# Optimization experiments

Hardware: AMD Instinct MI355X
Metric: run time of the kernel (lower is better)

## Reference

```python
import jax, jax.numpy as jnp
import numpy as np
from functools import partial

HID = 256
HOR = 5

def _lin(k, i, o):
    return jax.random.normal(k, (i, o), jnp.float32) / np.sqrt(i)

def setup_inputs() -> dict:
    key = jax.random.key(0)
    ks = jax.random.split(key, 32)
    B, T, D, Hf, Wf = 4, 16, 768, 16, 16
    H, W = 1024, 1024
    inp = {}
    inp['features'] = jax.random.normal(ks[0], (B, T, D, Hf, Wf), jnp.float32)
    inp['predictions'] = jax.random.uniform(ks[1], (B, T, 1, H, W), dtype=jnp.float32)
    # position encoder: 4 -> HID -> HID
    inp['pe_w1'] = _lin(ks[2], 4, HID); inp['pe_b1'] = jnp.zeros((HID,), jnp.float32)
    inp['pe_w2'] = _lin(ks[3], HID, HID); inp['pe_b2'] = jnp.zeros((HID,), jnp.float32)
    # 2-layer LSTM, gate order i,f,g,o (torch convention)
    inp['wih0'] = _lin(ks[4], HID, 4 * HID); inp['whh0'] = _lin(ks[5], HID, 4 * HID)
    inp['bih0'] = jnp.zeros((4 * HID,), jnp.float32); inp['bhh0'] = jnp.zeros((4 * HID,), jnp.float32)
    inp['wih1'] = _lin(ks[6], HID, 4 * HID); inp['whh1'] = _lin(ks[7], HID, 4 * HID)
    inp['bih1'] = jnp.zeros((4 * HID,), jnp.float32); inp['bhh1'] = jnp.zeros((4 * HID,), jnp.float32)
    # motion predictor: HID -> HID -> HID/2 -> HOR*4
    inp['mp_w1'] = _lin(ks[8], HID, HID); inp['mp_b1'] = jnp.zeros((HID,), jnp.float32)
    inp['mp_w2'] = _lin(ks[9], HID, HID // 2); inp['mp_b2'] = jnp.zeros((HID // 2,), jnp.float32)
    inp['mp_w3'] = _lin(ks[10], HID // 2, HOR * 4); inp['mp_b3'] = jnp.zeros((HOR * 4,), jnp.float32)
    # confidence: HID -> HID/2 -> HOR
    inp['cf_w1'] = _lin(ks[11], HID, HID // 2); inp['cf_b1'] = jnp.zeros((HID // 2,), jnp.float32)
    inp['cf_w2'] = _lin(ks[12], HID // 2, HOR); inp['cf_b2'] = jnp.zeros((HOR,), jnp.float32)
    return inp

def _extract_bboxes(predictions):
    # predictions: (B,T,1,H,W) -> bboxes (B,T,4) in (cx,cy,w,h), normalized
    B, T, _, H, W = predictions.shape
    mask = predictions[:, :, 0] > 0.5  # (B,T,H,W)
    xs = jnp.arange(W, dtype=jnp.float32)           # (W,)
    ys = jnp.arange(H, dtype=jnp.float32)[:, None]  # (H,1)
    big = jnp.float32(H + W)
    x_min = jnp.min(jnp.where(mask, xs, big), axis=(-2, -1))
    x_max = jnp.max(jnp.where(mask, xs, -1.0), axis=(-2, -1))
    y_min = jnp.min(jnp.where(mask, ys, big), axis=(-2, -1))
    y_max = jnp.max(jnp.where(mask, ys, -1.0), axis=(-2, -1))
    has = jnp.any(mask, axis=(-2, -1))  # (B,T)
    cx = (x_min + x_max) / 2.0 / W
    cy = (y_min + y_max) / 2.0 / H
    w = (x_max - x_min) / W
    h = (y_max - y_min) / H
    bbox = jnp.stack([cx, cy, w, h], axis=-1)  # (B,T,4)
    default = jnp.array([0.5, 0.5, 0.1, 0.1], dtype=jnp.float32)
    return jnp.where(has[..., None], bbox, default)

def _lstm_layer(x, wih, whh, bih, bhh):
    # x: (B,T,HID); returns (hs (B,T,H), h_final (B,H))
    B = x.shape[0]
    xg = jnp.einsum('bti,ig->btg', x, wih) + bih  # (B,T,4H)
    def step(carry, xg_t):
        h, c = carry
        g = xg_t + h @ whh + bhh
        i, f, gg, o = jnp.split(g, 4, axis=-1)
        i = jax.nn.sigmoid(i); f = jax.nn.sigmoid(f)
        gg = jnp.tanh(gg); o = jax.nn.sigmoid(o)
        c = f * c + i * gg
        h = o * jnp.tanh(c)
        return (h, c), h
    z = jnp.zeros((B, HID), x.dtype)
    (h, c), hs = jax.lax.scan(step, (z, z), xg.swapaxes(0, 1))
    return hs.swapaxes(0, 1), h

def reference(features, predictions, pe_w1, pe_b1, pe_w2, pe_b2,
              wih0, whh0, bih0, bhh0, wih1, whh1, bih1, bhh1,
              mp_w1, mp_b1, mp_w2, mp_b2, mp_w3, mp_b3,
              cf_w1, cf_b1, cf_w2, cf_b2):
    B, T = features.shape[:2]
    bboxes = _extract_bboxes(predictions)  # (B,T,4)
    pos = jax.nn.relu(bboxes @ pe_w1 + pe_b1)
    pos = jax.nn.relu(pos @ pe_w2 + pe_b2)  # (B,T,HID)
    h1, _ = _lstm_layer(pos, wih0, whh0, bih0, bhh0)
    motion_features, last_hidden = _lstm_layer(h1, wih1, whh1, bih1, bhh1)
    x = jax.nn.relu(last_hidden @ mp_w1 + mp_b1)
    x = jax.nn.relu(x @ mp_w2 + mp_b2)
    predicted_deltas = (x @ mp_w3 + mp_b3).reshape(B, HOR, 4)
    last_bbox = bboxes[:, -1:, :]
    predicted_bboxes = last_bbox + jnp.cumsum(predicted_deltas, axis=1)
    c = jax.nn.relu(last_hidden @ cf_w1 + cf_b1)
    confidence = jax.nn.sigmoid(c @ cf_w2 + cf_b2)  # (B,HOR)
    predicted_locations = predicted_bboxes[..., :2]
    predicted_scales = predicted_bboxes[..., 2:]
    return (predicted_deltas, predicted_bboxes, predicted_locations,
            predicted_scales, motion_features, confidence, bboxes)
```

## Files before the change

### kernel.cpp

```cpp
#include <hip/hip_runtime.h>
#include <math.h>

#define BIGI (1 << 30)

#define PM_OFF    0
#define MM_OFF    8192
#define FLAGS_OFF 8448
#define POS2_OFF  8512
#define H1S_OFF   24896
#define H2_OFF    41280

#define OUT_DELTAS 0
#define OUT_PBB    80
#define OUT_LOC    160
#define OUT_SCL    200
#define OUT_MF     240
#define OUT_CONF   16624
#define OUT_BBOX   16644

__device__ __forceinline__ float sigmoidf_(float x) { return 1.0f / (1.0f + expf(-x)); }

__device__ __forceinline__ void cstoref(float* p, float v) {
    __hip_atomic_store(p, v, __ATOMIC_RELAXED, __HIP_MEMORY_SCOPE_AGENT);
}
__device__ __forceinline__ float cloadf(const float* p) {
    return __hip_atomic_load(p, __ATOMIC_RELAXED, __HIP_MEMORY_SCOPE_AGENT);
}
__device__ __forceinline__ int cloadi(const int* p) {
    return __hip_atomic_load(p, __ATOMIC_RELAXED, __HIP_MEMORY_SCOPE_AGENT);
}

__device__ __forceinline__ void pollf(const int* fl, int target) {
    if (threadIdx.x == 0) {
        for (;;) {
            int m = cloadi(fl + 0);
            m = min(m, cloadi(fl + 1)); m = min(m, cloadi(fl + 2));
            m = min(m, cloadi(fl + 3)); m = min(m, cloadi(fl + 4));
            m = min(m, cloadi(fl + 5)); m = min(m, cloadi(fl + 6));
            m = min(m, cloadi(fl + 7));
            if (m >= target) break;
            __builtin_amdgcn_s_sleep(2);
        }
    }
    __syncthreads();
}

__global__ __launch_bounds__(256) void k_minmax(const float4* __restrict__ pred,
                                                int* __restrict__ pm) {
    int img = blockIdx.x >> 5;
    int chunk = blockIdx.x & 31;
    int tid = threadIdx.x;
    int base = img * 262144 + chunk * 8192 + tid;
    int xmn = BIGI, xmx = -1, ymn = BIGI, ymx = -1;
#pragma unroll 4
    for (int i = 0; i < 32; ++i) {
        int idx4 = base + i * 256;
        float4 v = pred[idx4];
        int x = (idx4 << 2) & 1023;
        int y = (idx4 >> 8) & 1023;
        bool m0 = v.x > 0.5f, m1 = v.y > 0.5f, m2 = v.z > 0.5f, m3 = v.w > 0.5f;
        int cmn = m0 ? x : (m1 ? x + 1 : (m2 ? x + 2 : (m3 ? x + 3 : BIGI)));
        int cmx = m3 ? x + 3 : (m2 ? x + 2 : (m1 ? x + 1 : (m0 ? x : -1)));
        xmn = min(xmn, cmn);
        xmx = max(xmx, cmx);
        if (m0 | m1 | m2 | m3) { ymn = min(ymn, y); ymx = max(ymx, y); }
    }
    for (int off = 32; off > 0; off >>= 1) {
        xmn = min(xmn, __shfl_down(xmn, off));
        xmx = max(xmx, __shfl_down(xmx, off));
        ymn = min(ymn, __shfl_down(ymn, off));
        ymx = max(ymx, __shfl_down(ymx, off));
    }
    __shared__ int red[4][4];
    int wave = tid >> 6;
    if ((tid & 63) == 0) { red[0][wave] = xmn; red[1][wave] = xmx; red[2][wave] = ymn; red[3][wave] = ymx; }
    __syncthreads();
    if (tid == 0) {
        xmn = min(min(red[0][0], red[0][1]), min(red[0][2], red[0][3]));
        xmx = max(max(red[1][0], red[1][1]), max(red[1][2], red[1][3]));
        ymn = min(min(red[2][0], red[2][1]), min(red[2][2], red[2][3]));
        ymx = max(max(red[3][0], red[3][1]), max(red[3][2], red[3][3]));
        ((int4*)pm)[blockIdx.x] = make_int4(xmn, xmx, ymn, ymx);
    }
}

__global__ __launch_bounds__(256) void k_prep(const int* __restrict__ pm,
    int* __restrict__ mm, int* __restrict__ flags,
    const float* __restrict__ pe_w1, const float* __restrict__ pe_b1,
    const float* __restrict__ pe_w2, const float* __restrict__ pe_b2,
    float* __restrict__ pos2, float* __restrict__ out) {
    __shared__ float bb[4];
    __shared__ float p1[256];
    int w = blockIdx.x, tid = threadIdx.x;
    if (w == 0 && tid < 64) flags[tid] = 0;
    if (tid < 64) {
        int xmn = BIGI, xmx = -1, ymn = BIGI, ymx = -1;
        if (tid < 32) {
            int4 v = ((const int4*)pm)[w * 32 + tid];
            xmn = v.x; xmx = v.y; ymn = v.z; ymx = v.w;
        }
        for (int off = 32; off > 0; off >>= 1) {
            xmn = min(xmn, __shfl_down(xmn, off));
            xmx = max(xmx, __shfl_down(xmx, off));
            ymn = min(ymn, __shfl_down(ymn, off));
            ymx = max(ymx, __shfl_down(ymx, off));
        }
        if (tid == 0) {
            mm[w * 4 + 0] = xmn; mm[w * 4 + 1] = xmx;
            mm[w * 4 + 2] = ymn; mm[w * 4 + 3] = ymx;
            float cx, cy, bw, bh;
            if (xmx >= 0) {
                cx = (float)(xmn + xmx) * (0.5f / 1024.0f);
                cy = (float)(ymn + ymx) * (0.5f / 1024.0f);
                bw = (float)(xmx - xmn) * (1.0f / 1024.0f);
                bh = (float)(ymx - ymn) * (1.0f / 1024.0f);
            } else { cx = 0.5f; cy = 0.5f; bw = 0.1f; bh = 0.1f; }
            bb[0] = cx; bb[1] = cy; bb[2] = bw; bb[3] = bh;
            out[OUT_BBOX + w * 4 + 0] = cx; out[OUT_BBOX + w * 4 + 1] = cy;
            out[OUT_BBOX + w * 4 + 2] = bw; out[OUT_BBOX + w * 4 + 3] = bh;
        }
    }
    __syncthreads();
    {
        float v = bb[0] * pe_w1[tid] + bb[1] * pe_w1[256 + tid] +
                  bb[2] * pe_w1[512 + tid] + bb[3] * pe_w1[768 + tid] + pe_b1[tid];
        p1[tid] = fmaxf(v, 0.0f);
    }
    __syncthreads();
    float acc = pe_b2[tid];
#pragma unroll 4
    for (int k = 0; k < 256; ++k) acc += p1[k] * pe_w2[k * 256 + tid];
    pos2[w * 256 + tid] = fmaxf(acc, 0.0f);
}

__global__ __launch_bounds__(256, 1) void k_lstm(
    const float* __restrict__ wih0, const float* __restrict__ whh0,
    const float* __restrict__ bih0, const float* __restrict__ bhh0,
    const float* __restrict__ wih1, const float* __restrict__ whh1,
    const float* __restrict__ bih1, const float* __restrict__ bhh1,
    const float* __restrict__ mp_w1, const float* __restrict__ mp_b1,
    const float* __restrict__ mp_w2, const float* __restrict__ mp_b2,
    const float* __restrict__ mp_w3, const float* __restrict__ mp_b3,
    const float* __restrict__ cf_w1, const float* __restrict__ cf_b1,
    const float* __restrict__ cf_w2, const float* __restrict__ cf_b2,
    const float* __restrict__ pos2, float* __restrict__ h1s,
    float* __restrict__ h2, int* __restrict__ flags,
    const int* __restrict__ mm, float* __restrict__ out) {
    __shared__ float px[4096];
    __shared__ float partX[4096];
    __shared__ float xgl[2048];
    __shared__ float hsm[256];
    __shared__ float part[256];
    __shared__ float gatesL[128];
    const int tid = threadIdx.x;
    const int b = blockIdx.x >> 3, g = blockIdx.x & 7;
    const int j = tid & 127, kh = tid >> 7;
    const int col = ((j >> 5) << 8) + g * 32 + (j & 31);
    int* flb = flags + b * 16;
    float4 wreg[32];

    for (int layer = 0; layer < 2; ++layer) {
        const float* wih = layer ? wih1 : wih0;
        const float* whh = layer ? whh1 : whh0;
        const float* bih = layer ? bih1 : bih0;
        const float* bhh = layer ? bhh1 : bhh0;

        if (layer == 0) {
            for (int i = tid; i < 4096; i += 256) px[i] = pos2[b * 4096 + i];
        } else {
            pollf(flb, 16);
            for (int i = tid; i < 4096; i += 256) px[i] = cloadf(&h1s[b * 4096 + i]);
        }
#pragma unroll
        for (int k4 = 0; k4 < 32; ++k4) {
            int r = kh * 128 + k4 * 4;
            wreg[k4].x = wih[(r + 0) * 1024 + col];
            wreg[k4].y = wih[(r + 1) * 1024 + col];
            wreg[k4].z = wih[(r + 2) * 1024 + col];
            wreg[k4].w = wih[(r + 3) * 1024 + col];
        }
        __syncthreads();
        for (int t = 0; t < 16; ++t) {
            float a = 0.0f;
            const float4* p4 = (const float4*)&px[t * 256 + kh * 128];
#pragma unroll
            for (int k4 = 0; k4 < 32; ++k4) {
                float4 h4 = p4[k4];
                a += h4.x * wreg[k4].x + h4.y * wreg[k4].y + h4.z * wreg[k4].z + h4.w * wreg[k4].w;
            }
            partX[kh * 2048 + t * 128 + j] = a;
        }
        __syncthreads();
        {
            float bsum = bih[col] + bhh[col];
            int t0 = tid >> 7;
            for (int i = 0; i < 8; ++i) {
                int t = t0 + 2 * i;
                xgl[t * 128 + j] = partX[t * 128 + j] + partX[2048 + t * 128 + j] + bsum;
            }
        }
#pragma unroll
        for (int k4 = 0; k4 < 32; ++k4) {
            int r = kh * 128 + k4 * 4;
            wreg[k4].x = whh[(r + 0) * 1024 + col];
            wreg[k4].y = whh[(r + 1) * 1024 + col];
            wreg[k4].z = whh[(r + 2) * 1024 + col];
            wreg[k4].w = whh[(r + 3) * 1024 + col];
        }
        __syncthreads();

        float cst = 0.0f;
        for (int t = 0; t < 16; ++t) {
            if (t) {
                pollf(flb, layer * 16 + t);
                hsm[tid] = (layer == 0)
                    ? cloadf(&h1s[(b * 16 + t - 1) * 256 + tid])
                    : cloadf(&h2[b * 512 + ((t - 1) & 1) * 256 + tid]);
            }
            __syncthreads();
            float a = 0.0f;
            if (t) {
                const float4* h4p = (const float4*)&hsm[kh * 128];
#pragma unroll
                for (int k4 = 0; k4 < 32; ++k4) {
                    float4 h4 = h4p[k4];
                    a += h4.x * wreg[k4].x + h4.y * wreg[k4].y + h4.z * wreg[k4].z + h4.w * wreg[k4].w;
                }
            }
            part[tid] = a;
            __syncthreads();
            if (tid < 128) gatesL[tid] = part[tid] + part[128 + tid] + xgl[t * 128 + tid];
            __syncthreads();
            if (tid < 32) {
                float gi = gatesL[tid], gf = gatesL[32 + tid];
                float gg = gatesL[64 + tid], go = gatesL[96 + tid];
                float i_ = sigmoidf_(gi), f_ = sigmoidf_(gf);
                float g_ = tanhf(gg), o_ = sigmoidf_(go);
                cst = f_ * cst + i_ * g_;
                float h = o_ * tanhf(cst);
                int unit = g * 32 + tid;
                if (layer == 0) {
                    cstoref(&h1s[(b * 16 + t) * 256 + unit], h);
                } else {
                    cstoref(&h2[b * 512 + (t & 1) * 256 + unit], h);
                    out[OUT_MF + (b * 16 + t) * 256 + unit] = h;
                }
            }
            __syncthreads();
            if (tid == 0)
                __hip_atomic_store(&flb[g], layer * 16 + t + 1,
                                   __ATOMIC_RELAXED, __HIP_MEMORY_SCOPE_AGENT);
        }
    }

    if (g != 0) return;
    pollf(flb, 32);
    float* lh = px;
    float* x1 = px + 256;
    float* c1 = px + 512;
    float* x2 = px + 768;
    float* dl = px + 896;
    lh[tid] = cloadf(&h2[b * 512 + 256 + tid]);
    __syncthreads();
    {
        float a = mp_b1[tid];
#pragma unroll 4
        for (int k = 0; k < 256; ++k) a += lh[k] * mp_w1[k * 256 + tid];
        x1[tid] = fmaxf(a, 0.0f);
    }
    if (tid < 128) {
        float a = cf_b1[tid];
#pragma unroll 4
        for (int k = 0; k < 256; ++k) a += lh[k] * cf_w1[k * 128 + tid];
        c1[tid] = fmaxf(a, 0.0f);
    }
    __syncthreads();
    if (tid < 128) {
        float a = mp_b2[tid];
#pragma unroll 4
        for (int k = 0; k < 256; ++k) a += x1[k] * mp_w2[k * 128 + tid];
        x2[tid] = fmaxf(a, 0.0f);
    } else if (tid < 133) {
        int jj = tid - 128;
        float a = cf_b2[jj];
#pragma unroll 4
        for (int k = 0; k < 128; ++k) a += c1[k] * cf_w2[k * 5 + jj];
        out[OUT_CONF + b * 5 + jj] = sigmoidf_(a);
    }
    __syncthreads();
    if (tid < 20) {
        float a = mp_b3[tid];
#pragma unroll 4
        for (int k = 0; k < 128; ++k) a += x2[k] * mp_w3[k * 20 + tid];
        dl[tid] = a;
        out[OUT_DELTAS + b * 20 + tid] = a;
    }
    __syncthreads();
    if (tid < 4) {
        int img = b * 16 + 15;
        int xmn = mm[img * 4 + 0], xmx = mm[img * 4 + 1];
        int ymn = mm[img * 4 + 2], ymx = mm[img * 4 + 3];
        float v;
        if (xmx >= 0) {
            if (tid == 0)      v = (float)(xmn + xmx) * (0.5f / 1024.0f);
            else if (tid == 1) v = (float)(ymn + ymx) * (0.5f / 1024.0f);
            else if (tid == 2) v = (float)(xmx - xmn) * (1.0f / 1024.0f);
            else               v = (float)(ymx - ymn) * (1.0f / 1024.0f);
        } else v = (tid < 2) ? 0.5f : 0.1f;
        float acc = v;
        for (int hh = 0; hh < 5; ++hh) {
            acc += dl[hh * 4 + tid];
            out[OUT_PBB + b * 20 + hh * 4 + tid] = acc;
            if (tid < 2) out[OUT_LOC + b * 10 + hh * 2 + tid] = acc;
            else out[OUT_SCL + b * 10 + hh * 2 + (tid - 2)] = acc;
        }
    }
}

extern "C" void kernel_launch(void* const* d_in, const int* in_sizes, int n_in,
                              void* d_out, int out_size, void* d_ws, size_t ws_size,
                              hipStream_t stream) {
    (void)in_sizes; (void)n_in; (void)out_size; (void)ws_size;
    const float* pred = (const float*)d_in[1];
    const float* pe_w1 = (const float*)d_in[2];
    const float* pe_b1 = (const float*)d_in[3];
    const float* pe_w2 = (const float*)d_in[4];
    const float* pe_b2 = (const float*)d_in[5];
    const float* wih0 = (const float*)d_in[6];
    const float* whh0 = (const float*)d_in[7];
    const float* bih0 = (const float*)d_in[8];
    const float* bhh0 = (const float*)d_in[9];
    const float* wih1 = (const float*)d_in[10];
    const float* whh1 = (const float*)d_in[11];
    const float* bih1 = (const float*)d_in[12];
    const float* bhh1 = (const float*)d_in[13];
    const float* mp_w1 = (const float*)d_in[14];
    const float* mp_b1 = (const float*)d_in[15];
    const float* mp_w2 = (const float*)d_in[16];
    const float* mp_b2 = (const float*)d_in[17];
    const float* mp_w3 = (const float*)d_in[18];
    const float* mp_b3 = (const float*)d_in[19];
    const float* cf_w1 = (const float*)d_in[20];
    const float* cf_b1 = (const float*)d_in[21];
    const float* cf_w2 = (const float*)d_in[22];
    const float* cf_b2 = (const float*)d_in[23];
    float* out = (float*)d_out;
    int* wsi = (int*)d_ws;
    float* wsf = (float*)d_ws;

    hipLaunchKernelGGL(k_minmax, dim3(64 * 32), dim3(256), 0, stream,
                       (const float4*)pred, wsi + PM_OFF);
    hipLaunchKernelGGL(k_prep, dim3(64), dim3(256), 0, stream,
                       wsi + PM_OFF, wsi + MM_OFF, wsi + FLAGS_OFF,
                       pe_w1, pe_b1, pe_w2, pe_b2,
                       wsf + POS2_OFF, out);
    hipLaunchKernelGGL(k_lstm, dim3(32), dim3(256), 0, stream,
                       wih0, whh0, bih0, bhh0,
                       wih1, whh1, bih1, bhh1,
                       mp_w1, mp_b1, mp_w2, mp_b2, mp_w3, mp_b3,
                       cf_w1, cf_b1, cf_w2, cf_b2,
                       wsf + POS2_OFF, wsf + H1S_OFF, wsf + H2_OFF,
                       wsi + FLAGS_OFF, wsi + MM_OFF, out);
}
```

Baseline: 681.7 us.

## Replace per-block flag polling with tagged 64-bit hidden-state words

Inter-block synchronization in the recurrent LSTM no longer uses separate per-group progress flags. Each hidden value is written as one 64-bit word that packs the value with a step tag, and consumers spin on each word until the tag matches. This removes the extra __syncthreads and flag store per step, and the single-thread poll followed by a barrier before the loads. In exchange every thread polls its own word, the zeroing of the larger tagged buffer moves into the prep kernel, and hidden-state traffic doubles in size.

New measurement: 658.2 us. 3.5% less time.

```diff
diff --git a/kernel.cpp b/kernel.cpp
--- a/kernel.cpp
+++ b/kernel.cpp
@@ -5,10 +5,10 @@
 
 #define PM_OFF    0
 #define MM_OFF    8192
-#define FLAGS_OFF 8448
-#define POS2_OFF  8512
-#define H1S_OFF   24896
-#define H2_OFF    41280
+#define POS2_OFF  8448
+#define HT0_OFF   24832
+#define HT2_OFF   57600
+#define HT_WORDS  36864
 
 #define OUT_DELTAS 0
 #define OUT_PBB    80
@@ -20,29 +20,18 @@
 
 __device__ __forceinline__ float sigmoidf_(float x) { return 1.0f / (1.0f + expf(-x)); }
 
-__device__ __forceinline__ void cstoref(float* p, float v) {
+__device__ __forceinline__ void storeh(unsigned long long* p, float h, int tag) {
+    unsigned long long v =
+        ((unsigned long long)(unsigned)tag << 32) | (unsigned long long)__float_as_uint(h);
     __hip_atomic_store(p, v, __ATOMIC_RELAXED, __HIP_MEMORY_SCOPE_AGENT);
 }
-__device__ __forceinline__ float cloadf(const float* p) {
-    return __hip_atomic_load(p, __ATOMIC_RELAXED, __HIP_MEMORY_SCOPE_AGENT);
-}
-__device__ __forceinline__ int cloadi(const int* p) {
-    return __hip_atomic_load(p, __ATOMIC_RELAXED, __HIP_MEMORY_SCOPE_AGENT);
-}
-
-__device__ __forceinline__ void pollf(const int* fl, int target) {
-    if (threadIdx.x == 0) {
-        for (;;) {
-            int m = cloadi(fl + 0);
-            m = min(m, cloadi(fl + 1)); m = min(m, cloadi(fl + 2));
-            m = min(m, cloadi(fl + 3)); m = min(m, cloadi(fl + 4));
-            m = min(m, cloadi(fl + 5)); m = min(m, cloadi(fl + 6));
-            m = min(m, cloadi(fl + 7));
-            if (m >= target) break;
-            __builtin_amdgcn_s_sleep(2);
-        }
-    }
-    __syncthreads();
+__device__ __forceinline__ float pollh(const unsigned long long* p, int tag) {
+    unsigned long long v = __hip_atomic_load(p, __ATOMIC_RELAXED, __HIP_MEMORY_SCOPE_AGENT);
+    while ((int)(v >> 32) != tag) {
+        __builtin_amdgcn_s_sleep(1);
+        v = __hip_atomic_load(p, __ATOMIC_RELAXED, __HIP_MEMORY_SCOPE_AGENT);
+    }
+    return __uint_as_float((unsigned)v);
 }
 
 __global__ __launch_bounds__(256) void k_minmax(const float4* __restrict__ pred,
@@ -85,14 +74,14 @@
 }
 
 __global__ __launch_bounds__(256) void k_prep(const int* __restrict__ pm,
-    int* __restrict__ mm, int* __restrict__ flags,
+    int* __restrict__ mm, int* __restrict__ ht,
     const float* __restrict__ pe_w1, const float* __restrict__ pe_b1,
     const float* __restrict__ pe_w2, const float* __restrict__ pe_b2,
     float* __restrict__ pos2, float* __restrict__ out) {
     __shared__ float bb[4];
     __shared__ float p1[256];
     int w = blockIdx.x, tid = threadIdx.x;
-    if (w == 0 && tid < 64) flags[tid] = 0;
+    for (int i = w * 256 + tid; i < HT_WORDS; i += 64 * 256) ht[i] = 0;
     if (tid < 64) {
         int xmn = BIGI, xmx = -1, ymn = BIGI, ymx = -1;
         if (tid < 32) {
@@ -143,8 +132,8 @@
     const float* __restrict__ mp_w3, const float* __restrict__ mp_b3,
     const float* __restrict__ cf_w1, const float* __restrict__ cf_b1,
     const float* __restrict__ cf_w2, const float* __restrict__ cf_b2,
-    const float* __restrict__ pos2, float* __restrict__ h1s,
-    float* __restrict__ h2, int* __restrict__ flags,
+    const float* __restrict__ pos2, unsigned long long* __restrict__ hT0,
+    unsigned long long* __restrict__ hT2,
     const int* __restrict__ mm, float* __restrict__ out) {
     __shared__ float px[4096];
     __shared__ float partX[4096];
@@ -156,7 +145,6 @@
     const int b = blockIdx.x >> 3, g = blockIdx.x & 7;
     const int j = tid & 127, kh = tid >> 7;
     const int col = ((j >> 5) << 8) + g * 32 + (j & 31);
-    int* flb = flags + b * 16;
     float4 wreg[32];
 
     for (int layer = 0; layer < 2; ++layer) {
@@ -168,8 +156,10 @@
         if (layer == 0) {
             for (int i = tid; i < 4096; i += 256) px[i] = pos2[b * 4096 + i];
         } else {
-            pollf(flb, 16);
-            for (int i = tid; i < 4096; i += 256) px[i] = cloadf(&h1s[b * 4096 + i]);
+            for (int i = tid; i < 4096; i += 256) {
+                int t = i >> 8, unit = i & 255;
+                px[i] = pollh(&hT0[((b * 16 + t) << 8) + unit], t + 1);
+            }
         }
 #pragma unroll
         for (int k4 = 0; k4 < 32; ++k4) {
@@ -212,10 +202,10 @@
         float cst = 0.0f;
         for (int t = 0; t < 16; ++t) {
             if (t) {
-                pollf(flb, layer * 16 + t);
-                hsm[tid] = (layer == 0)
-                    ? cloadf(&h1s[(b * 16 + t - 1) * 256 + tid])
-                    : cloadf(&h2[b * 512 + ((t - 1) & 1) * 256 + tid]);
+                const unsigned long long* src = (layer == 0)
+                    ? &hT0[((b * 16 + (t - 1)) << 8) + tid]
+                    : &hT2[(((b << 1) | ((t - 1) & 1)) << 8) + tid];
+                hsm[tid] = pollh(src, layer * 16 + t);
             }
             __syncthreads();
             float a = 0.0f;
@@ -239,28 +229,25 @@
                 cst = f_ * cst + i_ * g_;
                 float h = o_ * tanhf(cst);
                 int unit = g * 32 + tid;
+                int tag = layer * 16 + t + 1;
                 if (layer == 0) {
-                    cstoref(&h1s[(b * 16 + t) * 256 + unit], h);
+                    storeh(&hT0[((b * 16 + t) << 8) + unit], h, tag);
                 } else {
-                    cstoref(&h2[b * 512 + (t & 1) * 256 + unit], h);
+                    storeh(&hT2[(((b << 1) | (t & 1)) << 8) + unit], h, tag);
                     out[OUT_MF + (b * 16 + t) * 256 + unit] = h;
                 }
             }
-            __syncthreads();
-            if (tid == 0)
-                __hip_atomic_store(&flb[g], layer * 16 + t + 1,
-                                   __ATOMIC_RELAXED, __HIP_MEMORY_SCOPE_AGENT);
         }
     }
 
     if (g != 0) return;
-    pollf(flb, 32);
+    __syncthreads();
     float* lh = px;
     float* x1 = px + 256;
     float* c1 = px + 512;
     float* x2 = px + 768;
     float* dl = px + 896;
-    lh[tid] = cloadf(&h2[b * 512 + 256 + tid]);
+    lh[tid] = pollh(&hT2[((b << 1) | 1) << 8 | tid], 32);
     __syncthreads();
     {
         float a = mp_b1[tid];
@@ -351,7 +338,7 @@
     hipLaunchKernelGGL(k_minmax, dim3(64 * 32), dim3(256), 0, stream,
                        (const float4*)pred, wsi + PM_OFF);
     hipLaunchKernelGGL(k_prep, dim3(64), dim3(256), 0, stream,
-                       wsi + PM_OFF, wsi + MM_OFF, wsi + FLAGS_OFF,
+                       wsi + PM_OFF, wsi + MM_OFF, wsi + HT0_OFF,
                        pe_w1, pe_b1, pe_w2, pe_b2,
                        wsf + POS2_OFF, out);
     hipLaunchKernelGGL(k_lstm, dim3(32), dim3(256), 0, stream,
@@ -359,6 +346,8 @@
                        wih1, whh1, bih1, bhh1,
                        mp_w1, mp_b1, mp_w2, mp_b2, mp_w3, mp_b3,
                        cf_w1, cf_b1, cf_w2, cf_b2,
-                       wsf + POS2_OFF, wsf + H1S_OFF, wsf + H2_OFF,
-                       wsi + FLAGS_OFF, wsi + MM_OFF, out);
-}
+                       wsf + POS2_OFF,
+                       (unsigned long long*)(wsi + HT0_OFF),
+                       (unsigned long long*)(wsi + HT2_OFF),
+                       wsi + MM_OFF, out);
+}
```
